# Performance work log

Measured on AMD Instinct MI355X. Metric: run time of the kernel, lower is better.

## Reference

```python
import jax, jax.numpy as jnp
import numpy as np

MOMENTUM = 0.05
EPS = 1e-06


def _gated_ema(x, g):
    """y[t] = (1 - g[t]) * y[t-1] + g[t] * x[t], y[-1] = 0.
    x: (B, C, T), g: (B, 1, T) -> (B, C, T)"""
    xT = jnp.moveaxis(x, -1, 0)  # (T, B, C)
    gT = jnp.moveaxis(g, -1, 0)  # (T, B, 1)
    init = jnp.zeros(x.shape[:-1], x.dtype)  # (B, C)

    def step(carry, inp):
        xt, gt = inp
        carry = (1.0 - gt) * carry + gt * xt
        return carry, carry

    _, ys = jax.lax.scan(step, init, (xT, gT))
    return jnp.moveaxis(ys, 0, -1)


def setup_inputs() -> dict:
    key = jax.random.key(0)
    ks = jax.random.split(key, 6)
    B, C, T = 8, 512, 8192
    return {
        "x": jax.random.normal(ks[0], (B, C, T), dtype=jnp.float32),
        "g": jax.random.uniform(ks[1], (B, 1, T), dtype=jnp.float32),
        "Wa_w": jax.random.normal(ks[2], (1, C, 1), dtype=jnp.float32),
        "Wb_w": jax.random.normal(ks[3], (1, C, 1), dtype=jnp.float32),
        "Wo_w": jax.random.normal(ks[4], (C, 1, 1), dtype=jnp.float32),
        "Wo_b": jax.random.normal(ks[5], (C,), dtype=jnp.float32),
    }


def reference(x, g, Wa_w, Wb_w, Wo_w, Wo_b):
    sg = jax.lax.stop_gradient
    C = x.shape[1]
    g = g * MOMENTUM  # time-varying momentum gate
    # Wa: 1x1 conv C->1 with softmax over input channels (convex combination)
    wa = jax.nn.softmax(Wa_w, axis=1)  # (1, C, 1)
    mean = jnp.sum(wa * _gated_ema(sg(x), g), axis=1, keepdims=True)  # (B, 1, T)
    xc = x - mean
    wb = jax.nn.softmax(Wb_w, axis=1)  # (1, C, 1)
    var = jnp.sum(wb * _gated_ema(jnp.square(sg(xc)), g), axis=1, keepdims=True)  # (B, 1, T)
    xn = xc / jnp.sqrt(var + EPS)
    # Wo: grouped 1x1 conv (groups=C) == per-channel scale + bias
    return xn * Wo_w.reshape(1, C, 1) + Wo_b.reshape(1, C, 1)
```

## Files before the change

kernel.cpp:

```cpp
#include <hip/hip_runtime.h>

constexpr int BB = 8, CC = 512, TT = 8192;
static_assert((TT & (TT - 1)) == 0 && (CC & (CC - 1)) == 0, "pow2");
constexpr int LOG_T = 13, LOG_C = 9;
constexpr float MOM = 0.05f, EPSV = 1e-6f;

__global__ __launch_bounds__(512) void k_softmax(const float* __restrict__ Wa,
                                                 const float* __restrict__ Wb,
                                                 float* __restrict__ wa,
                                                 float* __restrict__ wb) {
  __shared__ float red[512];
  const int tid = threadIdx.x;

  float v = Wa[tid];
  red[tid] = v; __syncthreads();
  for (int off = 256; off > 0; off >>= 1) {
    if (tid < off) red[tid] = fmaxf(red[tid], red[tid + off]);
    __syncthreads();
  }
  float mx = red[0]; __syncthreads();
  float e = expf(v - mx);
  red[tid] = e; __syncthreads();
  for (int off = 256; off > 0; off >>= 1) {
    if (tid < off) red[tid] += red[tid + off];
    __syncthreads();
  }
  wa[tid] = e / red[0];
  __syncthreads();

  v = Wb[tid];
  red[tid] = v; __syncthreads();
  for (int off = 256; off > 0; off >>= 1) {
    if (tid < off) red[tid] = fmaxf(red[tid], red[tid + off]);
    __syncthreads();
  }
  mx = red[0]; __syncthreads();
  e = expf(v - mx);
  red[tid] = e; __syncthreads();
  for (int off = 256; off > 0; off >>= 1) {
    if (tid < off) red[tid] += red[tid + off];
    __syncthreads();
  }
  wb[tid] = e / red[0];
}

__global__ __launch_bounds__(256) void k_reduce_c(const float* __restrict__ x,
                                                  const float* __restrict__ wa,
                                                  const float* __restrict__ wb,
                                                  float* __restrict__ sa,
                                                  float* __restrict__ sb,
                                                  float* __restrict__ sb2) {
  __shared__ float lwa[CC];
  __shared__ float lwb[CC];
  __shared__ float red[3][4][256];
  const int tid = threadIdx.x;
  lwa[tid] = wa[tid]; lwa[tid + 256] = wa[tid + 256];
  lwb[tid] = wb[tid]; lwb[tid + 256] = wb[tid + 256];
  __syncthreads();

  const int tilesPerB = TT / 256;
  const int b = blockIdx.x / tilesPerB;
  const int tbase = (blockIdx.x % tilesPerB) * 256;
  const int l = tid & 63;
  const int cp = tid >> 6;
  const int t = tbase + l * 4;
  const float* xp = x + ((size_t)(b * CC + cp * 128)) * TT + t;

  float a0=0,a1=0,a2=0,a3=0;
  float b0=0,b1=0,b2=0,b3=0;
  float q0=0,q1=0,q2=0,q3=0;
  const int cbase = cp * 128;
  #pragma unroll 4
  for (int cc = 0; cc < 128; ++cc) {
    float4 xv = *(const float4*)(xp + (size_t)cc * TT);
    float wac = lwa[cbase + cc];
    float wbc = lwb[cbase + cc];
    a0 = fmaf(wac, xv.x, a0); a1 = fmaf(wac, xv.y, a1);
    a2 = fmaf(wac, xv.z, a2); a3 = fmaf(wac, xv.w, a3);
    b0 = fmaf(wbc, xv.x, b0); b1 = fmaf(wbc, xv.y, b1);
    b2 = fmaf(wbc, xv.z, b2); b3 = fmaf(wbc, xv.w, b3);
    q0 = fmaf(wbc * xv.x, xv.x, q0); q1 = fmaf(wbc * xv.y, xv.y, q1);
    q2 = fmaf(wbc * xv.z, xv.z, q2); q3 = fmaf(wbc * xv.w, xv.w, q3);
  }
  const int li = l * 4;
  red[0][cp][li+0]=a0; red[0][cp][li+1]=a1; red[0][cp][li+2]=a2; red[0][cp][li+3]=a3;
  red[1][cp][li+0]=b0; red[1][cp][li+1]=b1; red[1][cp][li+2]=b2; red[1][cp][li+3]=b3;
  red[2][cp][li+0]=q0; red[2][cp][li+1]=q1; red[2][cp][li+2]=q2; red[2][cp][li+3]=q3;
  __syncthreads();

  if (tid < 64) {
    const int o = tid * 4;
    float oa[4], ob[4], oq[4];
    #pragma unroll
    for (int k = 0; k < 4; ++k) {
      oa[k] = red[0][0][o+k] + red[0][1][o+k] + red[0][2][o+k] + red[0][3][o+k];
      ob[k] = red[1][0][o+k] + red[1][1][o+k] + red[1][2][o+k] + red[1][3][o+k];
      oq[k] = red[2][0][o+k] + red[2][1][o+k] + red[2][2][o+k] + red[2][3][o+k];
    }
    const size_t dst = (size_t)b * TT + tbase + o;
    *(float4*)(sa  + dst) = make_float4(oa[0], oa[1], oa[2], oa[3]);
    *(float4*)(sb  + dst) = make_float4(ob[0], ob[1], ob[2], ob[3]);
    *(float4*)(sb2 + dst) = make_float4(oq[0], oq[1], oq[2], oq[3]);
  }
}

__device__ __forceinline__ float affine_scan_prev(float A, float Bv, float* As,
                                                  float* Bs, int tid) {
  __syncthreads();
  As[tid] = A; Bs[tid] = Bv;
  __syncthreads();
  for (int off = 1; off < 256; off <<= 1) {
    float cA = As[tid], cB = Bs[tid];
    float pA = 1.f, pB = 0.f;
    if (tid >= off) { pA = As[tid - off]; pB = Bs[tid - off]; }
    __syncthreads();
    if (tid >= off) { As[tid] = cA * pA; Bs[tid] = fmaf(cA, pB, cB); }
    __syncthreads();
  }
  return (tid == 0) ? 0.f : Bs[tid - 1];
}

__global__ __launch_bounds__(256) void k_scan(const float* __restrict__ g,
                                              const float* __restrict__ sa,
                                              const float* __restrict__ sb,
                                              const float* __restrict__ sb2,
                                              float* __restrict__ mean,
                                              float* __restrict__ inv) {
  constexpr int CH = TT / 256;
  __shared__ float As[256], Bs[256];
  const int tid = threadIdx.x;
  const size_t base = (size_t)blockIdx.x * TT + (size_t)tid * CH;

  float gt[CH], pa[CH], mv[CH], vin[CH];

  float A = 1.f, Bv = 0.f;
  #pragma unroll
  for (int j = 0; j < CH; ++j) {
    float gg = g[base + j] * MOM;
    gt[j] = gg;
    pa[j] = gg * sa[base + j];
    float a = 1.f - gg;
    A *= a;
    Bv = fmaf(a, Bv, pa[j]);
  }
  float m = affine_scan_prev(A, Bv, As, Bs, tid);
  #pragma unroll
  for (int j = 0; j < CH; ++j) {
    m = fmaf(1.f - gt[j], m, pa[j]);
    mv[j] = m;
    mean[base + j] = m;
  }

  float A2 = 1.f, B2 = 0.f;
  #pragma unroll
  for (int j = 0; j < CH; ++j) {
    float sbv = sb[base + j], s2v = sb2[base + j];
    float vi = fmaf(mv[j], mv[j], fmaf(-2.f * mv[j], sbv, s2v));
    vin[j] = vi;
    float a = 1.f - gt[j];
    A2 *= a;
    B2 = fmaf(a, B2, gt[j] * vi);
  }
  float v = affine_scan_prev(A2, B2, As, Bs, tid);
  #pragma unroll
  for (int j = 0; j < CH; ++j) {
    v = fmaf(1.f - gt[j], v, gt[j] * vin[j]);
    inv[base + j] = rsqrtf(v + EPSV);
  }
}

__global__ __launch_bounds__(256) void k_out(const float* __restrict__ x,
                                             const float* __restrict__ mean,
                                             const float* __restrict__ inv,
                                             const float* __restrict__ wo,
                                             const float* __restrict__ bo,
                                             float* __restrict__ out) {
  const size_t n4 = (size_t)BB * CC * TT / 4;
  const size_t stride = (size_t)gridDim.x * blockDim.x;
  for (size_t i = (size_t)blockIdx.x * blockDim.x + threadIdx.x; i < n4; i += stride) {
    const size_t flat = i * 4;
    const int t = (int)(flat & (TT - 1));
    const size_t rem = flat >> LOG_T;
    const int c = (int)(rem & (CC - 1));
    const int b = (int)(rem >> LOG_C);
    float4 xv = *(const float4*)(x + flat);
    const size_t mi = ((size_t)b << LOG_T) + t;
    float4 m4 = *(const float4*)(mean + mi);
    float4 i4 = *(const float4*)(inv + mi);
    const float w = wo[c], bb = bo[c];
    float4 o;
    o.x = fmaf((xv.x - m4.x) * i4.x, w, bb);
    o.y = fmaf((xv.y - m4.y) * i4.y, w, bb);
    o.z = fmaf((xv.z - m4.z) * i4.z, w, bb);
    o.w = fmaf((xv.w - m4.w) * i4.w, w, bb);
    *(float4*)(out + flat) = o;
  }
}

extern "C" void kernel_launch(void* const* d_in, const int* in_sizes, int n_in,
                              void* d_out, int out_size, void* d_ws, size_t ws_size,
                              hipStream_t stream) {
  const float* x    = (const float*)d_in[0];
  const float* g    = (const float*)d_in[1];
  const float* Wa_w = (const float*)d_in[2];
  const float* Wb_w = (const float*)d_in[3];
  const float* Wo_w = (const float*)d_in[4];
  const float* Wo_b = (const float*)d_in[5];
  float* out = (float*)d_out;

  constexpr int BT = BB * TT;
  float* ws   = (float*)d_ws;
  float* wa   = ws;
  float* wb   = ws + CC;
  float* sa   = ws + 2 * CC;
  float* sb   = sa + BT;
  float* sb2  = sb + BT;
  float* mean = sb2 + BT;
  float* inv  = mean + BT;

  k_softmax<<<1, 512, 0, stream>>>(Wa_w, Wb_w, wa, wb);
  k_reduce_c<<<BB * (TT / 256), 256, 0, stream>>>(x, wa, wb, sa, sb, sb2);
  k_scan<<<BB, 256, 0, stream>>>(g, sa, sb, sb2, mean, inv);
  k_out<<<2048, 256, 0, stream>>>(x, mean, inv, Wo_w, Wo_b, out);
}
```

Baseline: 90.92 us.

## Fuse softmax into reduce kernel, warp-shuffle scans, vectorize scan I/O, nontemporal stores

Drops the separate softmax launch: every reduce block now computes both channel softmaxes itself with wavefront shuffles. The block-level affine scan in the scan kernel is replaced by a shuffle-based intra-wave scan plus a short serial combine across waves. The scan kernel also fuses the mean recurrence with the variance-input pass and uses float4 loads and stores, and the output kernel writes with nontemporal stores. This removes one launch and many barrier-heavy shared-memory steps, at the cost of redundant softmax work in each of the 256 reduce blocks.

```diff
diff --git a/kernel.cpp b/kernel.cpp
--- a/kernel.cpp
+++ b/kernel.cpp
@@ -5,71 +5,62 @@
 constexpr int LOG_T = 13, LOG_C = 9;
 constexpr float MOM = 0.05f, EPSV = 1e-6f;
 
-__global__ __launch_bounds__(512) void k_softmax(const float* __restrict__ Wa,
-                                                 const float* __restrict__ Wb,
-                                                 float* __restrict__ wa,
-                                                 float* __restrict__ wb) {
-  __shared__ float red[512];
-  const int tid = threadIdx.x;
-
-  float v = Wa[tid];
-  red[tid] = v; __syncthreads();
-  for (int off = 256; off > 0; off >>= 1) {
-    if (tid < off) red[tid] = fmaxf(red[tid], red[tid + off]);
-    __syncthreads();
-  }
-  float mx = red[0]; __syncthreads();
-  float e = expf(v - mx);
-  red[tid] = e; __syncthreads();
-  for (int off = 256; off > 0; off >>= 1) {
-    if (tid < off) red[tid] += red[tid + off];
-    __syncthreads();
-  }
-  wa[tid] = e / red[0];
-  __syncthreads();
-
-  v = Wb[tid];
-  red[tid] = v; __syncthreads();
-  for (int off = 256; off > 0; off >>= 1) {
-    if (tid < off) red[tid] = fmaxf(red[tid], red[tid + off]);
-    __syncthreads();
-  }
-  mx = red[0]; __syncthreads();
-  e = expf(v - mx);
-  red[tid] = e; __syncthreads();
-  for (int off = 256; off > 0; off >>= 1) {
-    if (tid < off) red[tid] += red[tid + off];
-    __syncthreads();
-  }
-  wb[tid] = e / red[0];
-}
+typedef float v4f __attribute__((ext_vector_type(4)));
 
 __global__ __launch_bounds__(256) void k_reduce_c(const float* __restrict__ x,
-                                                  const float* __restrict__ wa,
-                                                  const float* __restrict__ wb,
+                                                  const float* __restrict__ Wa,
+                                                  const float* __restrict__ Wb,
                                                   float* __restrict__ sa,
                                                   float* __restrict__ sb,
                                                   float* __restrict__ sb2) {
   __shared__ float lwa[CC];
   __shared__ float lwb[CC];
+  __shared__ float xw[8];
   __shared__ float red[3][4][256];
   const int tid = threadIdx.x;
-  lwa[tid] = wa[tid]; lwa[tid + 256] = wa[tid + 256];
-  lwb[tid] = wb[tid]; lwb[tid + 256] = wb[tid + 256];
+  const int lane = tid & 63;
+  const int wid = tid >> 6;
+
+  float va0 = Wa[tid], va1 = Wa[tid + 256];
+  float vb0 = Wb[tid], vb1 = Wb[tid + 256];
+  float ma = fmaxf(va0, va1), mb = fmaxf(vb0, vb1);
+  #pragma unroll
+  for (int off = 32; off > 0; off >>= 1) {
+    ma = fmaxf(ma, __shfl_down(ma, off, 64));
+    mb = fmaxf(mb, __shfl_down(mb, off, 64));
+  }
+  if (lane == 0) { xw[wid] = ma; xw[4 + wid] = mb; }
+  __syncthreads();
+  ma = fmaxf(fmaxf(xw[0], xw[1]), fmaxf(xw[2], xw[3]));
+  mb = fmaxf(fmaxf(xw[4], xw[5]), fmaxf(xw[6], xw[7]));
+  float ea0 = expf(va0 - ma), ea1 = expf(va1 - ma);
+  float eb0 = expf(vb0 - mb), eb1 = expf(vb1 - mb);
+  float sA = ea0 + ea1, sB = eb0 + eb1;
+  #pragma unroll
+  for (int off = 32; off > 0; off >>= 1) {
+    sA += __shfl_down(sA, off, 64);
+    sB += __shfl_down(sB, off, 64);
+  }
+  __syncthreads();
+  if (lane == 0) { xw[wid] = sA; xw[4 + wid] = sB; }
+  __syncthreads();
+  sA = xw[0] + xw[1] + xw[2] + xw[3];
+  sB = xw[4] + xw[5] + xw[6] + xw[7];
+  const float rA = 1.f / sA, rB = 1.f / sB;
+  lwa[tid] = ea0 * rA; lwa[tid + 256] = ea1 * rA;
+  lwb[tid] = eb0 * rB; lwb[tid + 256] = eb1 * rB;
   __syncthreads();
 
   const int tilesPerB = TT / 256;
   const int b = blockIdx.x / tilesPerB;
   const int tbase = (blockIdx.x % tilesPerB) * 256;
-  const int l = tid & 63;
-  const int cp = tid >> 6;
-  const int t = tbase + l * 4;
-  const float* xp = x + ((size_t)(b * CC + cp * 128)) * TT + t;
+  const int t = tbase + lane * 4;
+  const float* xp = x + ((size_t)(b * CC + wid * 128)) * TT + t;
 
   float a0=0,a1=0,a2=0,a3=0;
   float b0=0,b1=0,b2=0,b3=0;
   float q0=0,q1=0,q2=0,q3=0;
-  const int cbase = cp * 128;
+  const int cbase = wid * 128;
   #pragma unroll 4
   for (int cc = 0; cc < 128; ++cc) {
     float4 xv = *(const float4*)(xp + (size_t)cc * TT);
@@ -82,10 +73,10 @@
     q0 = fmaf(wbc * xv.x, xv.x, q0); q1 = fmaf(wbc * xv.y, xv.y, q1);
     q2 = fmaf(wbc * xv.z, xv.z, q2); q3 = fmaf(wbc * xv.w, xv.w, q3);
   }
-  const int li = l * 4;
-  red[0][cp][li+0]=a0; red[0][cp][li+1]=a1; red[0][cp][li+2]=a2; red[0][cp][li+3]=a3;
-  red[1][cp][li+0]=b0; red[1][cp][li+1]=b1; red[1][cp][li+2]=b2; red[1][cp][li+3]=b3;
-  red[2][cp][li+0]=q0; red[2][cp][li+1]=q1; red[2][cp][li+2]=q2; red[2][cp][li+3]=q3;
+  const int li = lane * 4;
+  red[0][wid][li+0]=a0; red[0][wid][li+1]=a1; red[0][wid][li+2]=a2; red[0][wid][li+3]=a3;
+  red[1][wid][li+0]=b0; red[1][wid][li+1]=b1; red[1][wid][li+2]=b2; red[1][wid][li+3]=b3;
+  red[2][wid][li+0]=q0; red[2][wid][li+1]=q1; red[2][wid][li+2]=q2; red[2][wid][li+3]=q3;
   __syncthreads();
 
   if (tid < 64) {
@@ -104,20 +95,25 @@
   }
 }
 
-__device__ __forceinline__ float affine_scan_prev(float A, float Bv, float* As,
-                                                  float* Bs, int tid) {
-  __syncthreads();
-  As[tid] = A; Bs[tid] = Bv;
-  __syncthreads();
-  for (int off = 1; off < 256; off <<= 1) {
-    float cA = As[tid], cB = Bs[tid];
-    float pA = 1.f, pB = 0.f;
-    if (tid >= off) { pA = As[tid - off]; pB = Bs[tid - off]; }
-    __syncthreads();
-    if (tid >= off) { As[tid] = cA * pA; Bs[tid] = fmaf(cA, pB, cB); }
-    __syncthreads();
-  }
-  return (tid == 0) ? 0.f : Bs[tid - 1];
+__device__ __forceinline__ float affine_scan_prev(float A, float B, int tid,
+                                                  float* wAs, float* wBs) {
+  const int lane = tid & 63;
+  const int wid = tid >> 6;
+  #pragma unroll
+  for (int off = 1; off < 64; off <<= 1) {
+    float pA = __shfl_up(A, off, 64);
+    float pB = __shfl_up(B, off, 64);
+    if (lane >= off) { B = fmaf(A, pB, B); A *= pA; }
+  }
+  __syncthreads();
+  if (lane == 63) { wAs[wid] = A; wBs[wid] = B; }
+  __syncthreads();
+  float cB = 0.f;
+  for (int w = 0; w < wid; ++w) cB = fmaf(wAs[w], cB, wBs[w]);
+  float leA = __shfl_up(A, 1, 64);
+  float leB = __shfl_up(B, 1, 64);
+  if (lane == 0) { leA = 1.f; leB = 0.f; }
+  return fmaf(leA, cB, leB);
 }
 
 __global__ __launch_bounds__(256) void k_scan(const float* __restrict__ g,
@@ -127,45 +123,60 @@
                                               float* __restrict__ mean,
                                               float* __restrict__ inv) {
   constexpr int CH = TT / 256;
-  __shared__ float As[256], Bs[256];
+  __shared__ float wAs[4], wBs[4];
   const int tid = threadIdx.x;
   const size_t base = (size_t)blockIdx.x * TT + (size_t)tid * CH;
 
-  float gt[CH], pa[CH], mv[CH], vin[CH];
+  float gt[CH], pa[CH];
 
   float A = 1.f, Bv = 0.f;
   #pragma unroll
-  for (int j = 0; j < CH; ++j) {
-    float gg = g[base + j] * MOM;
-    gt[j] = gg;
-    pa[j] = gg * sa[base + j];
-    float a = 1.f - gg;
-    A *= a;
-    Bv = fmaf(a, Bv, pa[j]);
-  }
-  float m = affine_scan_prev(A, Bv, As, Bs, tid);
-  #pragma unroll
-  for (int j = 0; j < CH; ++j) {
-    m = fmaf(1.f - gt[j], m, pa[j]);
-    mv[j] = m;
-    mean[base + j] = m;
-  }
+  for (int j = 0; j < CH; j += 4) {
+    float gv[4]; *(float4*)gv = *(const float4*)(g + base + j);
+    float sv[4]; *(float4*)sv = *(const float4*)(sa + base + j);
+    #pragma unroll
+    for (int k = 0; k < 4; ++k) {
+      float gg = gv[k] * MOM;
+      gt[j + k] = gg;
+      float p = gg * sv[k];
+      pa[j + k] = p;
+      float a = 1.f - gg;
+      A *= a;
+      Bv = fmaf(a, Bv, p);
+    }
+  }
+  float m = affine_scan_prev(A, Bv, tid, wAs, wBs);
 
   float A2 = 1.f, B2 = 0.f;
   #pragma unroll
-  for (int j = 0; j < CH; ++j) {
-    float sbv = sb[base + j], s2v = sb2[base + j];
-    float vi = fmaf(mv[j], mv[j], fmaf(-2.f * mv[j], sbv, s2v));
-    vin[j] = vi;
-    float a = 1.f - gt[j];
-    A2 *= a;
-    B2 = fmaf(a, B2, gt[j] * vi);
-  }
-  float v = affine_scan_prev(A2, B2, As, Bs, tid);
-  #pragma unroll
-  for (int j = 0; j < CH; ++j) {
-    v = fmaf(1.f - gt[j], v, gt[j] * vin[j]);
-    inv[base + j] = rsqrtf(v + EPSV);
+  for (int j = 0; j < CH; j += 4) {
+    float bv[4]; *(float4*)bv = *(const float4*)(sb  + base + j);
+    float qv[4]; *(float4*)qv = *(const float4*)(sb2 + base + j);
+    float m4[4];
+    #pragma unroll
+    for (int k = 0; k < 4; ++k) {
+      float a = 1.f - gt[j + k];
+      m = fmaf(a, m, pa[j + k]);
+      m4[k] = m;
+      float vi = fmaf(m, m, fmaf(-2.f * m, bv[k], qv[k]));
+      float pv = gt[j + k] * vi;
+      pa[j + k] = pv;
+      A2 *= a;
+      B2 = fmaf(a, B2, pv);
+    }
+    *(float4*)(mean + base + j) = *(float4*)m4;
+  }
+  float v = affine_scan_prev(A2, B2, tid, wAs, wBs);
+
+  #pragma unroll
+  for (int j = 0; j < CH; j += 4) {
+    float i4[4];
+    #pragma unroll
+    for (int k = 0; k < 4; ++k) {
+      v = fmaf(1.f - gt[j + k], v, pa[j + k]);
+      i4[k] = rsqrtf(v + EPSV);
+    }
+    *(float4*)(inv + base + j) = *(float4*)i4;
   }
 }
 
@@ -188,12 +199,12 @@
     float4 m4 = *(const float4*)(mean + mi);
     float4 i4 = *(const float4*)(inv + mi);
     const float w = wo[c], bb = bo[c];
-    float4 o;
+    v4f o;
     o.x = fmaf((xv.x - m4.x) * i4.x, w, bb);
     o.y = fmaf((xv.y - m4.y) * i4.y, w, bb);
     o.z = fmaf((xv.z - m4.z) * i4.z, w, bb);
     o.w = fmaf((xv.w - m4.w) * i4.w, w, bb);
-    *(float4*)(out + flat) = o;
+    __builtin_nontemporal_store(o, (v4f*)(out + flat));
   }
 }
 
@@ -210,16 +221,13 @@
 
   constexpr int BT = BB * TT;
   float* ws   = (float*)d_ws;
-  float* wa   = ws;
-  float* wb   = ws + CC;
-  float* sa   = ws + 2 * CC;
+  float* sa   = ws;
   float* sb   = sa + BT;
   float* sb2  = sb + BT;
   float* mean = sb2 + BT;
   float* inv  = mean + BT;
 
-  k_softmax<<<1, 512, 0, stream>>>(Wa_w, Wb_w, wa, wb);
-  k_reduce_c<<<BB * (TT / 256), 256, 0, stream>>>(x, wa, wb, sa, sb, sb2);
+  k_reduce_c<<<BB * (TT / 256), 256, 0, stream>>>(x, Wa_w, Wb_w, sa, sb, sb2);
   k_scan<<<BB, 256, 0, stream>>>(g, sa, sb, sb2, mean, inv);
   k_out<<<2048, 256, 0, stream>>>(x, mean, inv, Wo_w, Wo_b, out);
 }
```

New measurement: 83.13 us. -8.6%, faster.
